# Kernel tuning notes

Measured on AMD Instinct MI355X. Metric: run time of the kernel, lower is better.

## Reference

```python
import jax, jax.numpy as jnp
import numpy as np

NEG_INF = -9e15  # matches the torch module's zero_vec constant
ALPHA = 0.2      # LeakyReLU negative slope


def setup_inputs() -> dict:
    key = jax.random.key(0)
    k1, k2, k3, k4, k5, k6 = jax.random.split(key, 6)
    N_t, N_o, F_in, F_out = 8192, 8192, 256, 64
    return {
        "t_input": jax.random.normal(k1, (N_t, F_in), dtype=jnp.float32),
        "o_input": jax.random.normal(k2, (N_o, F_in), dtype=jnp.float32),
        "W_t": jax.random.normal(k3, (F_in, F_out), dtype=jnp.float32) * 0.1,
        "W_o": jax.random.normal(k4, (F_in, F_out), dtype=jnp.float32) * 0.1,
        "a": jax.random.normal(k5, (2 * F_out, 1), dtype=jnp.float32) * 0.1,
        "adj": jax.random.randint(k6, (N_t, N_o), 0, 2, dtype=jnp.int32),
    }


def reference(t_input, o_input, W_t, W_o, a, adj):
    # Linear projections
    h_t = t_input @ W_t            # [N_t, F]
    h_o = o_input @ W_o            # [N_o, F]
    F_out = h_t.shape[1]
    a_t = a[:F_out, 0]             # [F]
    a_o = a[F_out:, 0]             # [F]
    # e[i,j] = leakyrelu(cat(h_t[i], h_o[j]) . a) = leakyrelu(h_t[i].a_t + h_o[j].a_o)
    # (avoids materializing the N_t*N_o*2F concat tensor; same math)
    e = jax.nn.leaky_relu(
        (h_t @ a_t)[:, None] + (h_o @ a_o)[None, :], negative_slope=ALPHA
    )                              # [N_t, N_o]
    attention = jnp.where(adj > 0, e, NEG_INF)
    attention = jax.nn.softmax(attention, axis=1)
    # dropout is identity at eval time
    h_prime = attention @ h_o      # [N_t, F]
    return jax.nn.elu(h_prime)     # concat=True
```

## Files before the change

### kernel.cpp

```cpp
#include <hip/hip_runtime.h>
#include <math.h>

#define NT 8192
#define NO 8192
#define FIN 256
#define FOUT 64
#define SPLIT 4
#define JS (NO/SPLIT)
#define ROWT 64
#define TJ 64

#define OFF_HO  ((size_t)0)
#define OFF_ST  (OFF_HO + (size_t)NO*FOUT)
#define OFF_SO  (OFF_ST + (size_t)NT)
#define OFF_WT  (OFF_SO + (size_t)NO)
#define OFF_WO  (OFF_WT + (size_t)FIN)
#define OFF_NUM (OFF_WO + (size_t)FIN)
#define OFF_DEN (OFF_NUM + (size_t)SPLIT*NT*FOUT)

__global__ void k_wvec(const float* __restrict__ Wt, const float* __restrict__ Wo,
                       const float* __restrict__ a, float* __restrict__ ws) {
  int k = threadIdx.x;
  float s1 = 0.f, s2 = 0.f;
#pragma unroll
  for (int fq = 0; fq < FOUT/4; ++fq) {
    float4 wt4 = *(const float4*)(Wt + (size_t)k*FOUT + fq*4);
    float4 wo4 = *(const float4*)(Wo + (size_t)k*FOUT + fq*4);
    float4 at4 = *(const float4*)(a + fq*4);
    float4 ao4 = *(const float4*)(a + FOUT + fq*4);
    s1 += wt4.x*at4.x + wt4.y*at4.y + wt4.z*at4.z + wt4.w*at4.w;
    s2 += wo4.x*ao4.x + wo4.y*ao4.y + wo4.z*ao4.z + wo4.w*ao4.w;
  }
  ws[OFF_WT + k] = s1;
  ws[OFF_WO + k] = s2;
}

__global__ void k_st(const float* __restrict__ tin, float* __restrict__ ws) {
  int lane = threadIdx.x & 63;
  int wv   = threadIdx.x >> 6;
  int row  = blockIdx.x * 4 + wv;
  float4 v = ((const float4*)(tin + (size_t)row*FIN))[lane];
  float4 w = ((const float4*)(ws + OFF_WT))[lane];
  float p = v.x*w.x + v.y*w.y + v.z*w.z + v.w*w.w;
#pragma unroll
  for (int m = 32; m >= 1; m >>= 1) p += __shfl_xor(p, m, 64);
  if (lane == 0) ws[OFF_ST + row] = p;
}

__global__ void k_ho(const float* __restrict__ oin, const float* __restrict__ Wo,
                     const float* __restrict__ a, float* __restrict__ ws) {
  int lane = threadIdx.x & 63;
  int wv = __builtin_amdgcn_readfirstlane(threadIdx.x >> 6);
  int r0 = blockIdx.x * 32 + wv * 8;
  const float* ob = oin + (size_t)r0 * FIN;
  float acc[8];
#pragma unroll
  for (int r = 0; r < 8; ++r) acc[r] = 0.f;
#pragma unroll 2
  for (int k = 0; k < FIN; k += 4) {
    float w0 = Wo[(size_t)(k+0)*FOUT + lane];
    float w1 = Wo[(size_t)(k+1)*FOUT + lane];
    float w2 = Wo[(size_t)(k+2)*FOUT + lane];
    float w3 = Wo[(size_t)(k+3)*FOUT + lane];
#pragma unroll
    for (int r = 0; r < 8; ++r) {
      float4 ov = *(const float4*)(ob + (size_t)r*FIN + k);
      acc[r] = fmaf(ov.x, w0, acc[r]);
      acc[r] = fmaf(ov.y, w1, acc[r]);
      acc[r] = fmaf(ov.z, w2, acc[r]);
      acc[r] = fmaf(ov.w, w3, acc[r]);
    }
  }
  float ao = a[FOUT + lane];
#pragma unroll
  for (int r = 0; r < 8; ++r) {
    ws[OFF_HO + (size_t)(r0 + r)*FOUT + lane] = acc[r];
    float p = acc[r] * ao;
#pragma unroll
    for (int m = 32; m >= 1; m >>= 1) p += __shfl_xor(p, m, 64);
    if (lane == 0) ws[OFF_SO + r0 + r] = p;
  }
}

__launch_bounds__(256, 2)
__global__ void k_attn(const int* __restrict__ adj, float* __restrict__ ws) {
  const float* st = ws + OFF_ST;
  const float* so = ws + OFF_SO;
  const float* ho = ws + OFF_HO;
  float* gnum = ws + OFF_NUM;
  float* gden = ws + OFF_DEN;

  __shared__ float sT[ROWT];
  __shared__ __align__(16) float sO[JS];
  __shared__ __align__(16) float wT[TJ][68];
  __shared__ __align__(16) float hT[TJ][68];
  __shared__ float denp[ROWT][16];

  int t  = threadIdx.x;
  int bx = blockIdx.x;
  int s  = bx & (SPLIT - 1);
  int bi = bx >> 2;
  int i0 = bi * ROWT;
  int jbase = s * JS;

  if (t < ROWT) sT[t] = st[i0 + t];
#pragma unroll
  for (int q = 0; q < JS/1024; ++q) {
    int u = q*256 + t;
    ((float4*)sO)[u] = ((const float4*)(so + jbase))[u];
  }
#pragma unroll
  for (int q = 0; q < 4; ++q) ((float*)denp)[q*256 + t] = 0.f;

  float acc[8][8];
#pragma unroll
  for (int r = 0; r < 8; ++r)
#pragma unroll
    for (int f = 0; f < 8; ++f) acc[r][f] = 0.f;

  int wv = t >> 6, lane = t & 63;
  int ig = lane >> 3, fg = lane & 7;

  for (int tt = 0; tt < JS/TJ; ++tt) {
    int j0 = jbase + tt*TJ;
    __syncthreads();
#pragma unroll
    for (int q = 0; q < 4; ++q) {
      int u = q*256 + t;
      int il = u >> 4, cs = u & 15;
      const int4 av = *(const int4*)(adj + (size_t)(i0 + il)*NO + j0 + cs*4);
      float sti = sT[il];
      int ob = tt*TJ + cs*4;
      float x0 = sti + sO[ob+0]; x0 = fmaxf(x0, 0.2f*x0);
      float x1 = sti + sO[ob+1]; x1 = fmaxf(x1, 0.2f*x1);
      float x2 = sti + sO[ob+2]; x2 = fmaxf(x2, 0.2f*x2);
      float x3 = sti + sO[ob+3]; x3 = fmaxf(x3, 0.2f*x3);
      float w0 = (av.x > 0) ? __expf(x0) : 0.f;
      float w1 = (av.y > 0) ? __expf(x1) : 0.f;
      float w2 = (av.z > 0) ? __expf(x2) : 0.f;
      float w3 = (av.w > 0) ? __expf(x3) : 0.f;
      wT[cs*4+0][il] = w0;
      wT[cs*4+1][il] = w1;
      wT[cs*4+2][il] = w2;
      wT[cs*4+3][il] = w3;
      denp[il][cs] += w0 + w1 + w2 + w3;
    }
#pragma unroll
    for (int q = 0; q < 4; ++q) {
      int u = q*256 + t;
      int jl = u >> 4, fs = u & 15;
      *(float4*)&hT[jl][fs*4] = *(const float4*)(ho + (size_t)(j0 + jl)*FOUT + fs*4);
    }
    __syncthreads();
#pragma unroll 4
    for (int jj = 0; jj < 16; ++jj) {
      int jl = wv*16 + jj;
      float4 wa = *(const float4*)&wT[jl][ig*8];
      float4 wb = *(const float4*)&wT[jl][ig*8 + 4];
      float4 ha = *(const float4*)&hT[jl][fg*8];
      float4 hb = *(const float4*)&hT[jl][fg*8 + 4];
      float wr[8] = {wa.x, wa.y, wa.z, wa.w, wb.x, wb.y, wb.z, wb.w};
      float hr[8] = {ha.x, ha.y, ha.z, ha.w, hb.x, hb.y, hb.z, hb.w};
#pragma unroll
      for (int r = 0; r < 8; ++r)
#pragma unroll
        for (int f = 0; f < 8; ++f)
          acc[r][f] = fmaf(wr[r], hr[f], acc[r][f]);
    }
  }
  __syncthreads();
  for (int w = 0; w < 4; ++w) {
    if (wv == w) {
#pragma unroll
      for (int r = 0; r < 8; ++r) {
        float* p = &wT[ig*8 + r][fg*8];
        if (w == 0) {
#pragma unroll
          for (int f = 0; f < 8; ++f) p[f] = acc[r][f];
        } else {
#pragma unroll
          for (int f = 0; f < 8; ++f) p[f] += acc[r][f];
        }
      }
    }
    __syncthreads();
  }
#pragma unroll
  for (int q = 0; q < 4; ++q) {
    int u = q*256 + t;
    int il = u >> 4, fs = u & 15;
    *(float4*)(gnum + ((size_t)s*NT + i0 + il)*FOUT + fs*4) = *(const float4*)&wT[il][fs*4];
  }
  if (t < ROWT) {
    float d = 0.f;
#pragma unroll
    for (int cs = 0; cs < 16; ++cs) d += denp[t][cs];
    gden[(size_t)s*NT + i0 + t] = d;
  }
}

__global__ void k_comb(const float* __restrict__ ws, float* __restrict__ out) {
  int idx = blockIdx.x * 256 + threadIdx.x;
  int i = idx >> 6;
  float num = 0.f, den = 0.f;
#pragma unroll
  for (int s = 0; s < SPLIT; ++s) {
    num += ws[OFF_NUM + ((size_t)s*NT + i)*FOUT + (idx & 63)];
    den += ws[OFF_DEN + (size_t)s*NT + i];
  }
  float r = num / den;
  out[idx] = (r > 0.f) ? r : (__expf(r) - 1.f);
}

extern "C" void kernel_launch(void* const* d_in, const int* in_sizes, int n_in,
                              void* d_out, int out_size, void* d_ws, size_t ws_size,
                              hipStream_t stream) {
  const float* tin = (const float*)d_in[0];
  const float* oin = (const float*)d_in[1];
  const float* Wt  = (const float*)d_in[2];
  const float* Wo  = (const float*)d_in[3];
  const float* a   = (const float*)d_in[4];
  const int*   adj = (const int*)d_in[5];
  float* out = (float*)d_out;
  float* ws  = (float*)d_ws;

  hipLaunchKernelGGL(k_wvec, dim3(1),            dim3(256), 0, stream, Wt, Wo, a, ws);
  hipLaunchKernelGGL(k_st,   dim3(NT/4),         dim3(256), 0, stream, tin, ws);
  hipLaunchKernelGGL(k_ho,   dim3(NO/32),        dim3(256), 0, stream, oin, Wo, a, ws);
  hipLaunchKernelGGL(k_attn, dim3(NT/ROWT*SPLIT), dim3(256), 0, stream, adj, ws);
  hipLaunchKernelGGL(k_comb, dim3(NT*FOUT/256),  dim3(256), 0, stream, ws, out);
}
```

Measured before the change: 479.4 us.

## Use bf16 MFMA for attention-weighted aggregation with transposed bf16 h_o

```diff
diff --git a/kernel.cpp b/kernel.cpp
--- a/kernel.cpp
+++ b/kernel.cpp
@@ -10,13 +10,25 @@
 #define ROWT 64
 #define TJ 64
 
-#define OFF_HO  ((size_t)0)
-#define OFF_ST  (OFF_HO + (size_t)NO*FOUT)
+#define OFF_ST  ((size_t)0)
 #define OFF_SO  (OFF_ST + (size_t)NT)
 #define OFF_WT  (OFF_SO + (size_t)NO)
 #define OFF_WO  (OFF_WT + (size_t)FIN)
 #define OFF_NUM (OFF_WO + (size_t)FIN)
 #define OFF_DEN (OFF_NUM + (size_t)SPLIT*NT*FOUT)
+#define OFF_HOB (OFF_DEN + (size_t)SPLIT*NT)
+
+typedef __attribute__((ext_vector_type(8))) short short8;
+typedef __attribute__((ext_vector_type(4))) float float4v;
+
+static __device__ __forceinline__ unsigned short f2bf(float x) {
+  unsigned int u = __float_as_uint(x);
+  unsigned int r = (u + 0x7fffu + ((u >> 16) & 1u)) >> 16;
+  return (unsigned short)r;
+}
+static __device__ __forceinline__ float bf2f(unsigned short b) {
+  return __uint_as_float(((unsigned int)b) << 16);
+}
 
 __global__ void k_wvec(const float* __restrict__ Wt, const float* __restrict__ Wo,
                        const float* __restrict__ a, float* __restrict__ ws) {
@@ -49,6 +61,7 @@
 
 __global__ void k_ho(const float* __restrict__ oin, const float* __restrict__ Wo,
                      const float* __restrict__ a, float* __restrict__ ws) {
+  unsigned short* hob = (unsigned short*)(ws + OFF_HOB);
   int lane = threadIdx.x & 63;
   int wv = __builtin_amdgcn_readfirstlane(threadIdx.x >> 6);
   int r0 = blockIdx.x * 32 + wv * 8;
@@ -74,7 +87,7 @@
   float ao = a[FOUT + lane];
 #pragma unroll
   for (int r = 0; r < 8; ++r) {
-    ws[OFF_HO + (size_t)(r0 + r)*FOUT + lane] = acc[r];
+    hob[(size_t)lane*NO + r0 + r] = f2bf(acc[r]);
     float p = acc[r] * ao;
 #pragma unroll
     for (int m = 32; m >= 1; m >>= 1) p += __shfl_xor(p, m, 64);
@@ -86,14 +99,14 @@
 __global__ void k_attn(const int* __restrict__ adj, float* __restrict__ ws) {
   const float* st = ws + OFF_ST;
   const float* so = ws + OFF_SO;
-  const float* ho = ws + OFF_HO;
+  const unsigned short* hob = (const unsigned short*)(ws + OFF_HOB);
   float* gnum = ws + OFF_NUM;
   float* gden = ws + OFF_DEN;
 
   __shared__ float sT[ROWT];
   __shared__ __align__(16) float sO[JS];
-  __shared__ __align__(16) float wT[TJ][68];
-  __shared__ __align__(16) float hT[TJ][68];
+  __shared__ __align__(16) unsigned short wB[TJ][72];
+  __shared__ __align__(16) unsigned short hB[TJ][72];
   __shared__ float denp[ROWT][16];
 
   int t  = threadIdx.x;
@@ -112,14 +125,20 @@
 #pragma unroll
   for (int q = 0; q < 4; ++q) ((float*)denp)[q*256 + t] = 0.f;
 
-  float acc[8][8];
-#pragma unroll
-  for (int r = 0; r < 8; ++r)
-#pragma unroll
-    for (int f = 0; f < 8; ++f) acc[r][f] = 0.f;
-
   int wv = t >> 6, lane = t & 63;
-  int ig = lane >> 3, fg = lane & 7;
+  int iq = (wv >> 1) * 32;
+  int fq = (wv & 1) * 32;
+  int lm = lane & 15;
+  int lk = (lane >> 4) * 8;
+
+  float4v acc[2][2];
+#pragma unroll
+  for (int mi = 0; mi < 2; ++mi)
+#pragma unroll
+    for (int fi = 0; fi < 2; ++fi) acc[mi][fi] = (float4v)0.f;
+
+  int hf = t >> 2;
+  int hj = (t & 3) * 16;
 
   for (int tt = 0; tt < JS/TJ; ++tt) {
     int j0 = jbase + tt*TJ;
@@ -139,58 +158,42 @@
       float w1 = (av.y > 0) ? __expf(x1) : 0.f;
       float w2 = (av.z > 0) ? __expf(x2) : 0.f;
       float w3 = (av.w > 0) ? __expf(x3) : 0.f;
-      wT[cs*4+0][il] = w0;
-      wT[cs*4+1][il] = w1;
-      wT[cs*4+2][il] = w2;
-      wT[cs*4+3][il] = w3;
-      denp[il][cs] += w0 + w1 + w2 + w3;
-    }
-#pragma unroll
-    for (int q = 0; q < 4; ++q) {
-      int u = q*256 + t;
-      int jl = u >> 4, fs = u & 15;
-      *(float4*)&hT[jl][fs*4] = *(const float4*)(ho + (size_t)(j0 + jl)*FOUT + fs*4);
+      ushort4 wp;
+      wp.x = f2bf(w0); wp.y = f2bf(w1); wp.z = f2bf(w2); wp.w = f2bf(w3);
+      *(ushort4*)&wB[il][cs*4] = wp;
+      denp[il][cs] += bf2f(wp.x) + bf2f(wp.y) + bf2f(wp.z) + bf2f(wp.w);
+    }
+    {
+      const unsigned short* hg = hob + (size_t)hf*NO + j0 + hj;
+      int4 h0 = *(const int4*)(hg);
+      int4 h1 = *(const int4*)(hg + 8);
+      *(int4*)&hB[hf][hj]     = h0;
+      *(int4*)&hB[hf][hj + 8] = h1;
     }
     __syncthreads();
-#pragma unroll 4
-    for (int jj = 0; jj < 16; ++jj) {
-      int jl = wv*16 + jj;
-      float4 wa = *(const float4*)&wT[jl][ig*8];
-      float4 wb = *(const float4*)&wT[jl][ig*8 + 4];
-      float4 ha = *(const float4*)&hT[jl][fg*8];
-      float4 hb = *(const float4*)&hT[jl][fg*8 + 4];
-      float wr[8] = {wa.x, wa.y, wa.z, wa.w, wb.x, wb.y, wb.z, wb.w};
-      float hr[8] = {ha.x, ha.y, ha.z, ha.w, hb.x, hb.y, hb.z, hb.w};
-#pragma unroll
-      for (int r = 0; r < 8; ++r)
-#pragma unroll
-        for (int f = 0; f < 8; ++f)
-          acc[r][f] = fmaf(wr[r], hr[f], acc[r][f]);
+#pragma unroll
+    for (int kk = 0; kk < 2; ++kk) {
+      short8 a0 = *(const short8*)&wB[iq      + lm][kk*32 + lk];
+      short8 a1 = *(const short8*)&wB[iq + 16 + lm][kk*32 + lk];
+      short8 b0 = *(const short8*)&hB[fq      + lm][kk*32 + lk];
+      short8 b1 = *(const short8*)&hB[fq + 16 + lm][kk*32 + lk];
+      acc[0][0] = __builtin_amdgcn_mfma_f32_16x16x32_bf16(a0, b0, acc[0][0], 0, 0, 0);
+      acc[0][1] = __builtin_amdgcn_mfma_f32_16x16x32_bf16(a0, b1, acc[0][1], 0, 0, 0);
+      acc[1][0] = __builtin_amdgcn_mfma_f32_16x16x32_bf16(a1, b0, acc[1][0], 0, 0, 0);
+      acc[1][1] = __builtin_amdgcn_mfma_f32_16x16x32_bf16(a1, b1, acc[1][1], 0, 0, 0);
     }
   }
   __syncthreads();
-  for (int w = 0; w < 4; ++w) {
-    if (wv == w) {
-#pragma unroll
-      for (int r = 0; r < 8; ++r) {
-        float* p = &wT[ig*8 + r][fg*8];
-        if (w == 0) {
-#pragma unroll
-          for (int f = 0; f < 8; ++f) p[f] = acc[r][f];
-        } else {
-#pragma unroll
-          for (int f = 0; f < 8; ++f) p[f] += acc[r][f];
-        }
+#pragma unroll
+  for (int mi = 0; mi < 2; ++mi)
+#pragma unroll
+    for (int fi = 0; fi < 2; ++fi)
+#pragma unroll
+      for (int r = 0; r < 4; ++r) {
+        int i = i0 + iq + mi*16 + (lane >> 4)*4 + r;
+        int f = fq + fi*16 + lm;
+        gnum[((size_t)s*NT + i)*FOUT + f] = acc[mi][fi][r];
       }
-    }
-    __syncthreads();
-  }
-#pragma unroll
-  for (int q = 0; q < 4; ++q) {
-    int u = q*256 + t;
-    int il = u >> 4, fs = u & 15;
-    *(float4*)(gnum + ((size_t)s*NT + i0 + il)*FOUT + fs*4) = *(const float4*)&wT[il][fs*4];
-  }
   if (t < ROWT) {
     float d = 0.f;
 #pragma unroll
@@ -224,9 +227,9 @@
   float* out = (float*)d_out;
   float* ws  = (float*)d_ws;
 
-  hipLaunchKernelGGL(k_wvec, dim3(1),            dim3(256), 0, stream, Wt, Wo, a, ws);
-  hipLaunchKernelGGL(k_st,   dim3(NT/4),         dim3(256), 0, stream, tin, ws);
-  hipLaunchKernelGGL(k_ho,   dim3(NO/32),        dim3(256), 0, stream, oin, Wo, a, ws);
+  hipLaunchKernelGGL(k_wvec, dim3(1),             dim3(256), 0, stream, Wt, Wo, a, ws);
+  hipLaunchKernelGGL(k_st,   dim3(NT/4),          dim3(256), 0, stream, tin, ws);
+  hipLaunchKernelGGL(k_ho,   dim3(NO/32),         dim3(256), 0, stream, oin, Wo, a, ws);
   hipLaunchKernelGGL(k_attn, dim3(NT/ROWT*SPLIT), dim3(256), 0, stream, adj, ws);
-  hipLaunchKernelGGL(k_comb, dim3(NT*FOUT/256),  dim3(256), 0, stream, ws, out);
-}
+  hipLaunchKernelGGL(k_comb, dim3(NT*FOUT/256),   dim3(256), 0, stream, ws, out);
+}
```

Result: no change. 473.7 us (-1.2%).
